# Optimization experiments

Measured on AMD Instinct MI355X. Metric: run time of the kernel, lower is better.

## Reference

```python
import jax, jax.numpy as jnp
import numpy as np

EPS = 1e-5

def _segment_mean(src_feat, edge_index, num_targets):
    # src_feat: [Ns, D]; edge_index: [2, E] = [source_idx, target_idx]
    msgs = src_feat[edge_index[0]]                                   # [E, D] gather
    agg = jax.ops.segment_sum(msgs, edge_index[1], num_segments=num_targets)
    deg = jax.ops.segment_sum(jnp.ones((edge_index.shape[1],), src_feat.dtype),
                              edge_index[1], num_segments=num_targets)
    return agg / jnp.clip(deg, 1.0)[:, None]

def _layernorm(x, gamma, beta):
    mu = jnp.mean(x, axis=-1, keepdims=True)
    var = jnp.mean(jnp.square(x - mu), axis=-1, keepdims=True)
    return (x - mu) * jax.lax.rsqrt(var + EPS) * gamma + beta

def setup_inputs() -> dict:
    key = jax.random.key(0)
    ks = jax.random.split(key, 8)
    NU, NI, E, D = 50000, 50000, 300000, 256
    s = 1.0 / np.sqrt(D)
    return {
        "user_features": jax.random.normal(ks[0], (NU, D), jnp.float32),
        "item_features": jax.random.normal(ks[1], (NI, D), jnp.float32),
        "user_item_edge_index": jax.random.randint(ks[2], (2, E), 0, NI),
        "item_user_edge_index": jax.random.randint(ks[3], (2, E), 0, NU),
        "Wu": jax.random.uniform(ks[4], (D, D), jnp.float32, -s, s),
        "bu": jax.random.uniform(ks[5], (D,), jnp.float32, -s, s),
        "Wi": jax.random.uniform(ks[6], (D, D), jnp.float32, -s, s),
        "bi": jax.random.uniform(ks[7], (D,), jnp.float32, -s, s),
        "gamma": jnp.ones((D,), jnp.float32),
        "beta": jnp.zeros((D,), jnp.float32),
    }

def reference(user_features, item_features, user_item_edge_index, item_user_edge_index,
              Wu, bu, Wi, bi, gamma, beta):
    num_items = item_features.shape[0]
    num_users = user_features.shape[0]
    # messages into items come from users; into users come from items
    item_messages = _segment_mean(user_features, user_item_edge_index, num_items)
    user_messages = _segment_mean(item_features, item_user_edge_index, num_users)
    u_new = (user_features + user_messages) @ Wu + bu
    i_new = (item_features + item_messages) @ Wi + bi
    u_new = _layernorm(jax.nn.relu(u_new), gamma, beta)
    i_new = _layernorm(jax.nn.relu(i_new), gamma, beta)
    return (u_new, i_new)
```

## Files before the change

kernel.cpp:

```cpp
#include <hip/hip_runtime.h>
#include <hip/hip_bf16.h>

#define D 256
#define BM 64
#define LDA 264
#define LDAF 260
#define LDK 72

typedef __attribute__((ext_vector_type(8))) __bf16 bf16x8;
typedef __attribute__((ext_vector_type(4))) float f32x4;

__device__ __forceinline__ float bf2f(unsigned short u) {
    union { unsigned int i; float f; } c; c.i = ((unsigned int)u) << 16; return c.f;
}
__device__ __forceinline__ float bf2f_lo(unsigned int u) {
    union { unsigned int i; float f; } c; c.i = u << 16; return c.f;
}
__device__ __forceinline__ float bf2f_hi(unsigned int u) {
    union { unsigned int i; float f; } c; c.i = u & 0xffff0000u; return c.f;
}
__device__ __forceinline__ unsigned short f2bf(float f) {
    __hip_bfloat16 h = __float2bfloat16(f);
    return *reinterpret_cast<unsigned short*>(&h);
}
__device__ __forceinline__ unsigned int pack2(float lo, float hi) {
    return (unsigned int)f2bf(lo) | ((unsigned int)f2bf(hi) << 16);
}


__global__ void k_prep(const float* __restrict__ uf, const float* __restrict__ itf,
                       const float* __restrict__ Wu, const float* __restrict__ Wi,
                       unsigned short* __restrict__ feat_bf,
                       unsigned short* __restrict__ Wt_u, unsigned short* __restrict__ Wt_i,
                       const int* __restrict__ iu_e, int Eiu,
                       const int* __restrict__ ui_e, int Eui,
                       int* __restrict__ deg, int NU,
                       size_t nfU, size_t nfTot, int nbF) {
    int b = blockIdx.x;
    if (b < nbF) {
        size_t base = ((size_t)b * 256 + threadIdx.x) * 8;
        if (base < nfTot) {
            const float* s = (base < nfU) ? (uf + base) : (itf + (base - nfU));
            float4 f0 = *(const float4*)s;
            float4 f1 = *(const float4*)(s + 4);
            ushort4 o0, o1;
            o0.x = f2bf(f0.x); o0.y = f2bf(f0.y); o0.z = f2bf(f0.z); o0.w = f2bf(f0.w);
            o1.x = f2bf(f1.x); o1.y = f2bf(f1.y); o1.z = f2bf(f1.z); o1.w = f2bf(f1.w);
            ((ushort4*)(feat_bf + base))[0] = o0;
            ((ushort4*)(feat_bf + base))[1] = o1;
        }
    } else if (b < nbF + 512) {
        int b2 = b - nbF;
        const float* W = (b2 < 256) ? Wu : Wi;
        unsigned short* Wt = (b2 < 256) ? Wt_u : Wt_i;
        int k = b2 & 255;
        int c = threadIdx.x;
        Wt[(size_t)c * 256 + k] = f2bf(W[(size_t)k * 256 + c]);
    } else {
        int e = (b - nbF - 512) * 256 + threadIdx.x;
        if (e < Eiu) {
            atomicAdd(&deg[iu_e[Eiu + e]], 1);
        } else if (e < Eiu + Eui) {
            int e2 = e - Eiu;
            atomicAdd(&deg[NU + ui_e[Eui + e2]], 1);
        }
    }
}

__global__ void k_scan_block(const int* __restrict__ deg, int N,
                             int* __restrict__ rs, int* __restrict__ bsums) {
    __shared__ int s[1024];
    int base = blockIdx.x * 1024;
    int t = threadIdx.x;
    int v = (base + t < N) ? deg[base + t] : 0;
    s[t] = v;
    __syncthreads();
    for (int off = 1; off < 1024; off <<= 1) {
        int add = (t >= off) ? s[t - off] : 0;
        __syncthreads();
        s[t] += add;
        __syncthreads();
    }
    if (base + t < N) rs[base + t + 1] = s[t];
    if (t == 1023) bsums[blockIdx.x] = s[1023];
}

__global__ void k_scan_sums(int* __restrict__ bsums, int nb) {
    __shared__ int s[1024];
    int t = threadIdx.x;
    int v = (t < nb) ? bsums[t] : 0;
    s[t] = v;
    __syncthreads();
    for (int off = 1; off < 1024; off <<= 1) {
        int add = (t >= off) ? s[t - off] : 0;
        __syncthreads();
        s[t] += add;
        __syncthreads();
    }
    if (t < nb) bsums[t] = s[t] - v;
}

__global__ void k_finalize(int N, int* __restrict__ rs, int* __restrict__ cur,
                           const int* __restrict__ bsums) {
    int i = blockIdx.x * blockDim.x + threadIdx.x;
    if (i < N) {
        int v = rs[i + 1] + bsums[i >> 10];
        rs[i + 1] = v;
        cur[i + 1] = v;
    }
    if (i == 0) { rs[0] = 0; cur[0] = 0; }
}

__global__ void k_fill2(const int* __restrict__ iu_e, int Eiu,
                        const int* __restrict__ ui_e, int Eui,
                        int* __restrict__ cur, int NU,
                        int* __restrict__ csr) {
    int e = blockIdx.x * blockDim.x + threadIdx.x;
    if (e < Eiu) {
        int d = iu_e[Eiu + e];
        int p = atomicAdd(&cur[d], 1);
        csr[p] = iu_e[e];
    } else if (e < Eiu + Eui) {
        int e2 = e - Eiu;
        int d = ui_e[Eui + e2];
        int p = atomicAdd(&cur[NU + d], 1);
        csr[p] = ui_e[e2];
    }
}

__launch_bounds__(256)
__global__ void k_fused(const unsigned short* __restrict__ uf_bf,
                        const unsigned short* __restrict__ if_bf,
                        const unsigned short* __restrict__ Wt_u,
                        const unsigned short* __restrict__ Wt_i,
                        const int* __restrict__ rs, const int* __restrict__ csr,
                        const float* __restrict__ bu, const float* __restrict__ bi,
                        const float* __restrict__ gamma, const float* __restrict__ beta,
                        int NU, int NI, int nbU, float* __restrict__ out) {
    __shared__ __align__(16) __hip_bfloat16 As[BM][LDA];
    __shared__ float red_s[BM][4];
    __shared__ float red_q[BM][4];

    int b = blockIdx.x;
    bool isU = b < nbU;
    const unsigned short* srcT = isU ? if_bf : uf_bf;
    const unsigned short* tgtT = isU ? uf_bf : if_bf;
    const unsigned short* Wt   = isU ? Wt_u : Wt_i;
    const float* bias          = isU ? bu : bi;
    float* Y                   = isU ? out : out + (size_t)NU * D;
    int N                      = isU ? NU : NI;
    int row0 = (isU ? b : b - nbU) * BM;
    int wvBase = (isU ? 0 : NU) + row0;

    int t = threadIdx.x;
    int lane = t & 63;
    int w = t >> 6;
    int l15 = lane & 15;
    int l4 = lane >> 4;
    int half = lane >> 5;
    int hl = lane & 31;

    for (int it = 0; it < 8; ++it) {
        int lrow = (it * 4 + w) * 2 + half;
        int grow = row0 + lrow;
        if (grow < N) {
            int wv = wvBase + lrow;
            int s0 = rs[wv], s1 = rs[wv + 1];
            float a0[8] = {}, a1[8] = {}, a2[8] = {}, a3[8] = {};
            int i = s0;
            for (; i + 4 <= s1; i += 4) {
                int e0 = csr[i], e1 = csr[i + 1], e2 = csr[i + 2], e3 = csr[i + 3];
                uint4 r0 = ((const uint4*)(srcT + (size_t)e0 * D))[hl];
                uint4 r1 = ((const uint4*)(srcT + (size_t)e1 * D))[hl];
                uint4 r2 = ((const uint4*)(srcT + (size_t)e2 * D))[hl];
                uint4 r3 = ((const uint4*)(srcT + (size_t)e3 * D))[hl];
                a0[0] += bf2f_lo(r0.x); a0[1] += bf2f_hi(r0.x); a0[2] += bf2f_lo(r0.y); a0[3] += bf2f_hi(r0.y);
                a0[4] += bf2f_lo(r0.z); a0[5] += bf2f_hi(r0.z); a0[6] += bf2f_lo(r0.w); a0[7] += bf2f_hi(r0.w);
                a1[0] += bf2f_lo(r1.x); a1[1] += bf2f_hi(r1.x); a1[2] += bf2f_lo(r1.y); a1[3] += bf2f_hi(r1.y);
                a1[4] += bf2f_lo(r1.z); a1[5] += bf2f_hi(r1.z); a1[6] += bf2f_lo(r1.w); a1[7] += bf2f_hi(r1.w);
                a2[0] += bf2f_lo(r2.x); a2[1] += bf2f_hi(r2.x); a2[2] += bf2f_lo(r2.y); a2[3] += bf2f_hi(r2.y);
                a2[4] += bf2f_lo(r2.z); a2[5] += bf2f_hi(r2.z); a2[6] += bf2f_lo(r2.w); a2[7] += bf2f_hi(r2.w);
                a3[0] += bf2f_lo(r3.x); a3[1] += bf2f_hi(r3.x); a3[2] += bf2f_lo(r3.y); a3[3] += bf2f_hi(r3.y);
                a3[4] += bf2f_lo(r3.z); a3[5] += bf2f_hi(r3.z); a3[6] += bf2f_lo(r3.w); a3[7] += bf2f_hi(r3.w);
            }
            for (; i < s1; ++i) {
                int e0 = csr[i];
                uint4 r0 = ((const uint4*)(srcT + (size_t)e0 * D))[hl];
                a0[0] += bf2f_lo(r0.x); a0[1] += bf2f_hi(r0.x); a0[2] += bf2f_lo(r0.y); a0[3] += bf2f_hi(r0.y);
                a0[4] += bf2f_lo(r0.z); a0[5] += bf2f_hi(r0.z); a0[6] += bf2f_lo(r0.w); a0[7] += bf2f_hi(r0.w);
            }
            int cnt = s1 - s0;
            float inv = 1.0f / (float)(cnt > 0 ? cnt : 1);
            uint4 tv = ((const uint4*)(tgtT + (size_t)grow * D))[hl];
            float x0 = bf2f_lo(tv.x) + (a0[0] + a1[0] + a2[0] + a3[0]) * inv;
            float x1 = bf2f_hi(tv.x) + (a0[1] + a1[1] + a2[1] + a3[1]) * inv;
            float x2 = bf2f_lo(tv.y) + (a0[2] + a1[2] + a2[2] + a3[2]) * inv;
            float x3 = bf2f_hi(tv.y) + (a0[3] + a1[3] + a2[3] + a3[3]) * inv;
            float x4 = bf2f_lo(tv.z) + (a0[4] + a1[4] + a2[4] + a3[4]) * inv;
            float x5 = bf2f_hi(tv.z) + (a0[5] + a1[5] + a2[5] + a3[5]) * inv;
            float x6 = bf2f_lo(tv.w) + (a0[6] + a1[6] + a2[6] + a3[6]) * inv;
            float x7 = bf2f_hi(tv.w) + (a0[7] + a1[7] + a2[7] + a3[7]) * inv;
            uint4 o;
            o.x = pack2(x0, x1); o.y = pack2(x2, x3); o.z = pack2(x4, x5); o.w = pack2(x6, x7);
            *(uint4*)&As[lrow][hl * 8] = o;
        } else {
            uint4 z = {0, 0, 0, 0};
            *(uint4*)&As[lrow][hl * 8] = z;
        }
    }

    f32x4 acc[4][4];
    f32x4 zero = {0.f, 0.f, 0.f, 0.f};
    #pragma unroll
    for (int fr = 0; fr < 4; fr++)
        #pragma unroll
        for (int fc = 0; fc < 4; fc++)
            acc[fr][fc] = zero;

    __syncthreads();

    const uint4* Bg = (const uint4*)Wt;
    int colB = w * 64 + l15;
    #pragma unroll
    for (int ks8 = 0; ks8 < 8; ++ks8) {
        uint4 bq[4];
        #pragma unroll
        for (int fc = 0; fc < 4; ++fc)
            bq[fc] = Bg[(size_t)(colB + fc * 16) * 32 + ks8 * 4 + l4];
        bf16x8 af[4];
        #pragma unroll
        for (int fr = 0; fr < 4; ++fr)
            af[fr] = *(const bf16x8*)&As[fr * 16 + l15][ks8 * 32 + l4 * 8];
        #pragma unroll
        for (int fr = 0; fr < 4; ++fr)
            #pragma unroll
            for (int fc = 0; fc < 4; ++fc)
                acc[fr][fc] = __builtin_amdgcn_mfma_f32_16x16x32_bf16(
                    af[fr], *(bf16x8*)&bq[fc], acc[fr][fc], 0, 0, 0);
    }

    float bias_c[4], gam_c[4], bet_c[4];
    #pragma unroll
    for (int fc = 0; fc < 4; fc++) {
        int col = w * 64 + fc * 16 + l15;
        bias_c[fc] = bias[col];
        gam_c[fc]  = gamma[col];
        bet_c[fc]  = beta[col];
    }

    #pragma unroll
    for (int fr = 0; fr < 4; fr++) {
        #pragma unroll
        for (int r = 0; r < 4; r++) {
            int row = fr * 16 + l4 * 4 + r;
            float s = 0.f, q = 0.f;
            #pragma unroll
            for (int fc = 0; fc < 4; fc++) {
                float v = acc[fr][fc][r] + bias_c[fc];
                v = fmaxf(v, 0.f);
                acc[fr][fc][r] = v;
                s += v;
                q += v * v;
            }
            #pragma unroll
            for (int m = 1; m < 16; m <<= 1) {
                s += __shfl_xor(s, m);
                q += __shfl_xor(q, m);
            }
            if (l15 == 0) { red_s[row][w] = s; red_q[row][w] = q; }
        }
    }
    __syncthreads();

    float* AsF = (float*)&As[0][0];
    for (int h = 0; h < 2; ++h) {
        #pragma unroll
        for (int fr2 = 0; fr2 < 2; ++fr2) {
            int fr = h * 2 + fr2;
            #pragma unroll
            for (int r = 0; r < 4; ++r) {
                int row = fr * 16 + l4 * 4 + r;
                float s = red_s[row][0] + red_s[row][1] + red_s[row][2] + red_s[row][3];
                float q = red_q[row][0] + red_q[row][1] + red_q[row][2] + red_q[row][3];
                float mu  = s * (1.0f / 256.0f);
                float var = q * (1.0f / 256.0f) - mu * mu;
                float rstd = rsqrtf(var + 1e-5f);
                int lr = row - h * 32;
                #pragma unroll
                for (int fc = 0; fc < 4; ++fc) {
                    int col = w * 64 + fc * 16 + l15;
                    AsF[lr * LDAF + col] = (acc[fr][fc][r] - mu) * rstd * gam_c[fc] + bet_c[fc];
                }
            }
        }
        __syncthreads();
        #pragma unroll
        for (int j = 0; j < 8; ++j) {
            int r = j * 4 + w;
            int grow = row0 + h * 32 + r;
            if (grow < N) {
                float4 v = *(float4*)&AsF[r * LDAF + lane * 4];
                *(float4*)&Y[(size_t)grow * D + lane * 4] = v;
            }
        }
        __syncthreads();
    }
}


__global__ void k_hist(const int* __restrict__ dst, int E, int* __restrict__ deg) {
    int e = blockIdx.x * blockDim.x + threadIdx.x;
    if (e < E) atomicAdd(&deg[dst[e]], 1);
}

__global__ void k_finalize_rs(int N, int* __restrict__ rs, const int* __restrict__ bsums) {
    int i = blockIdx.x * blockDim.x + threadIdx.x;
    if (i < N) rs[i + 1] += bsums[i >> 10];
    if (i == 0) rs[0] = 0;
}

__global__ void k_fill(const int* __restrict__ src, const int* __restrict__ dst, int E,
                       const int* __restrict__ rs, int* __restrict__ cursor,
                       int* __restrict__ csr) {
    int e = blockIdx.x * blockDim.x + threadIdx.x;
    if (e < E) {
        int d = dst[e];
        int p = atomicAdd(&cursor[d], 1);
        csr[rs[d] + p] = src[e];
    }
}

__global__ void k_msg_x(const float* __restrict__ srcf, const float* __restrict__ tgtf,
                        const int* __restrict__ rs, const int* __restrict__ csr,
                        int N, float* __restrict__ xout) {
    int wave = (blockIdx.x * blockDim.x + threadIdx.x) >> 6;
    int lane = threadIdx.x & 63;
    if (wave >= N) return;
    int s0 = rs[wave], s1 = rs[wave + 1];
    float4 acc = make_float4(0.f, 0.f, 0.f, 0.f);
    for (int i = s0; i < s1; i++) {
        int s = csr[i];
        float4 f = *(const float4*)&srcf[(size_t)s * D + lane * 4];
        acc.x += f.x; acc.y += f.y; acc.z += f.z; acc.w += f.w;
    }
    int cnt = s1 - s0;
    float inv = 1.0f / (float)(cnt > 0 ? cnt : 1);
    float4 t = *(const float4*)&tgtf[(size_t)wave * D + lane * 4];
    float4 x;
    x.x = t.x + acc.x * inv;
    x.y = t.y + acc.y * inv;
    x.z = t.z + acc.z * inv;
    x.w = t.w + acc.w * inv;
    *(float4*)&xout[(size_t)wave * D + lane * 4] = x;
}

__global__ void k_wcvt(const float* __restrict__ W0, const float* __restrict__ W1,
                       __hip_bfloat16* __restrict__ Wt0, __hip_bfloat16* __restrict__ Wt1) {
    int b = blockIdx.x;
    const float* W = (b < 256) ? W0 : W1;
    __hip_bfloat16* Wt = (b < 256) ? Wt0 : Wt1;
    int k = b & 255;
    int c = threadIdx.x;
    Wt[(size_t)c * 256 + k] = __float2bfloat16(W[(size_t)k * 256 + c]);
}

__launch_bounds__(256)
__global__ void k_gemm_mfma_ln(const float* __restrict__ X,
                               const __hip_bfloat16* __restrict__ Wt,
                               const float* __restrict__ bias,
                               const float* __restrict__ gamma,
                               const float* __restrict__ beta,
                               int N, float* __restrict__ Y) {
    __shared__ __hip_bfloat16 As[BM][LDK];
    __shared__ __hip_bfloat16 Bs[D][LDK];
    __shared__ float red_s[BM][4];
    __shared__ float red_q[BM][4];

    int t = threadIdx.x;
    int lane = t & 63;
    int w = t >> 6;
    int l15 = lane & 15;
    int l4 = lane >> 4;
    int row0 = blockIdx.x * BM;

    f32x4 acc[4][4];
    f32x4 zero = {0.f, 0.f, 0.f, 0.f};
    #pragma unroll
    for (int fr = 0; fr < 4; fr++)
        #pragma unroll
        for (int fc = 0; fc < 4; fc++)
            acc[fr][fc] = zero;

    for (int k0 = 0; k0 < D; k0 += 64) {
        {
            int i = t >> 2;
            int kq = (t & 3) * 16;
            int r = row0 + i;
            float4 f[4];
            if (r < N) {
                const float4* p = (const float4*)&X[(size_t)r * D + k0 + kq];
                f[0] = p[0]; f[1] = p[1]; f[2] = p[2]; f[3] = p[3];
            } else {
                float4 z4 = make_float4(0.f, 0.f, 0.f, 0.f);
                f[0] = z4; f[1] = z4; f[2] = z4; f[3] = z4;
            }
            __hip_bfloat16 vb[16];
            #pragma unroll
            for (int q = 0; q < 4; q++) {
                vb[q * 4 + 0] = __float2bfloat16(f[q].x);
                vb[q * 4 + 1] = __float2bfloat16(f[q].y);
                vb[q * 4 + 2] = __float2bfloat16(f[q].z);
                vb[q * 4 + 3] = __float2bfloat16(f[q].w);
            }
            *(uint4*)&As[i][kq]     = *(uint4*)&vb[0];
            *(uint4*)&As[i][kq + 8] = *(uint4*)&vb[8];
        }
        #pragma unroll
        for (int pass = 0; pass < 4; pass++) {
            int c = pass * 64 + (t >> 2);
            int kq = (t & 3) * 16;
            const uint4* p = (const uint4*)&Wt[(size_t)c * D + k0 + kq];
            uint4 b0 = p[0], b1 = p[1];
            *(uint4*)&Bs[c][kq]     = b0;
            *(uint4*)&Bs[c][kq + 8] = b1;
        }
        __syncthreads();

        #pragma unroll
        for (int ks = 0; ks < 2; ks++) {
            bf16x8 af[4], bg[4];
            #pragma unroll
            for (int fr = 0; fr < 4; fr++)
                af[fr] = *(const bf16x8*)&As[fr * 16 + l15][ks * 32 + l4 * 8];
            #pragma unroll
            for (int fc = 0; fc < 4; fc++)
                bg[fc] = *(const bf16x8*)&Bs[w * 64 + fc * 16 + l15][ks * 32 + l4 * 8];
            #pragma unroll
            for (int fr = 0; fr < 4; fr++)
                #pragma unroll
                for (int fc = 0; fc < 4; fc++)
                    acc[fr][fc] = __builtin_amdgcn_mfma_f32_16x16x32_bf16(
                        af[fr], bg[fc], acc[fr][fc], 0, 0, 0);
        }
        __syncthreads();
    }

    float bias_c[4], gam_c[4], bet_c[4];
    #pragma unroll
    for (int fc = 0; fc < 4; fc++) {
        int col = w * 64 + fc * 16 + l15;
        bias_c[fc] = bias[col];
        gam_c[fc]  = gamma[col];
        bet_c[fc]  = beta[col];
    }

    #pragma unroll
    for (int fr = 0; fr < 4; fr++) {
        #pragma unroll
        for (int r = 0; r < 4; r++) {
            int row = fr * 16 + l4 * 4 + r;
            float s = 0.f, q = 0.f;
            #pragma unroll
            for (int fc = 0; fc < 4; fc++) {
                float v = acc[fr][fc][r] + bias_c[fc];
                v = fmaxf(v, 0.f);
                acc[fr][fc][r] = v;
                s += v;
                q += v * v;
            }
            #pragma unroll
            for (int m = 1; m < 16; m <<= 1) {
                s += __shfl_xor(s, m);
                q += __shfl_xor(q, m);
            }
            if (l15 == 0) { red_s[row][w] = s; red_q[row][w] = q; }
        }
    }
    __syncthreads();

    #pragma unroll
    for (int fr = 0; fr < 4; fr++) {
        #pragma unroll
        for (int r = 0; r < 4; r++) {
            int row = fr * 16 + l4 * 4 + r;
            int grow = row0 + row;
            if (grow >= N) continue;
            float s = red_s[row][0] + red_s[row][1] + red_s[row][2] + red_s[row][3];
            float q = red_q[row][0] + red_q[row][1] + red_q[row][2] + red_q[row][3];
            float mu  = s * (1.0f / 256.0f);
            float var = q * (1.0f / 256.0f) - mu * mu;
            float rstd = rsqrtf(var + 1e-5f);
            #pragma unroll
            for (int fc = 0; fc < 4; fc++) {
                int col = w * 64 + fc * 16 + l15;
                Y[(size_t)grow * D + col] = (acc[fr][fc][r] - mu) * rstd * gam_c[fc] + bet_c[fc];
            }
        }
    }
}


extern "C" void kernel_launch(void* const* d_in, const int* in_sizes, int n_in,
                              void* d_out, int out_size, void* d_ws, size_t ws_size,
                              hipStream_t stream) {
    const float* uf    = (const float*)d_in[0];
    const float* itf   = (const float*)d_in[1];
    const int*   ui_e  = (const int*)d_in[2];
    const int*   iu_e  = (const int*)d_in[3];
    const float* Wu    = (const float*)d_in[4];
    const float* bu    = (const float*)d_in[5];
    const float* Wi    = (const float*)d_in[6];
    const float* bi    = (const float*)d_in[7];
    const float* gamma = (const float*)d_in[8];
    const float* beta  = (const float*)d_in[9];

    int NU  = in_sizes[0] / D;
    int NI  = in_sizes[1] / D;
    int Eui = in_sizes[2] / 2;
    int Eiu = in_sizes[3] / 2;
    int Nmax = NU > NI ? NU : NI;
    int Ntot = NU + NI;
    int Etot = Eiu + Eui;

    float* out   = (float*)d_out;
    size_t nfU = (size_t)NU * D;
    size_t nfI = (size_t)NI * D;
    size_t nfTot = nfU + nfI;

    unsigned short* uf_bf = (unsigned short*)d_ws;
    unsigned short* if_bf = uf_bf + nfU;
    unsigned short* Wt_u2 = if_bf + nfI;
    unsigned short* Wt_i2 = Wt_u2 + 65536;
    int* deg2  = (int*)(Wt_i2 + 65536);
    int* rs2   = deg2 + Ntot;
    int* cur2  = rs2 + Ntot + 1;
    int* bsums = cur2 + Ntot + 1;
    int* csr2  = bsums + 1024;
    size_t needed = (size_t)((char*)(csr2 + Etot) - (char*)d_ws);

    if (ws_size >= needed) {
        int nbF = (int)((nfTot + 2047) / 2048);
        int nbH = (Etot + 255) / 256;
        hipMemsetAsync(deg2, 0, (size_t)Ntot * sizeof(int), stream);
        k_prep<<<nbF + 512 + nbH, 256, 0, stream>>>(uf, itf, Wu, Wi, uf_bf, Wt_u2, Wt_i2,
                                                    iu_e, Eiu, ui_e, Eui, deg2, NU,
                                                    nfU, nfTot, nbF);
        int nb = (Ntot + 1023) / 1024;
        k_scan_block<<<nb, 1024, 0, stream>>>(deg2, Ntot, rs2, bsums);
        k_scan_sums<<<1, 1024, 0, stream>>>(bsums, nb);
        k_finalize<<<(Ntot + 255) / 256, 256, 0, stream>>>(Ntot, rs2, cur2, bsums);
        k_fill2<<<nbH, 256, 0, stream>>>(iu_e, Eiu, ui_e, Eui, cur2, NU, csr2);
        int nbU = (NU + BM - 1) / BM;
        int nbI = (NI + BM - 1) / BM;
        k_fused<<<nbU + nbI, 256, 0, stream>>>(uf_bf, if_bf, Wt_u2, Wt_i2, rs2, csr2,
                                               bu, bi, gamma, beta, NU, NI, nbU, out);
        return;
    }

    float* u_out = out;
    float* i_out = out + nfU;
    __hip_bfloat16* Wt_u = (__hip_bfloat16*)d_ws;
    __hip_bfloat16* Wt_i = Wt_u + 256 * 256;
    int* deg    = (int*)(Wt_i + 256 * 256);
    int* rs     = deg + Nmax;
    int* bs     = rs + Nmax + 1;
    int* cursor = bs + 1024;
    int* csr    = cursor + Nmax;

    k_wcvt<<<512, 256, 0, stream>>>(Wu, Wi, Wt_u, Wt_i);

    auto run_side = [&](const float* srcf, const float* tgtf, const int* edges, int E,
                        int N, const __hip_bfloat16* Wt, const float* bias, float* y) {
        const int* esrc = edges;
        const int* edst = edges + E;
        hipMemsetAsync(deg, 0, (size_t)N * sizeof(int), stream);
        hipMemsetAsync(cursor, 0, (size_t)N * sizeof(int), stream);
        k_hist<<<(E + 255) / 256, 256, 0, stream>>>(edst, E, deg);
        int nb = (N + 1023) / 1024;
        k_scan_block<<<nb, 1024, 0, stream>>>(deg, N, rs, bs);
        k_scan_sums<<<1, 1024, 0, stream>>>(bs, nb);
        k_finalize_rs<<<(N + 255) / 256, 256, 0, stream>>>(N, rs, bs);
        k_fill<<<(E + 255) / 256, 256, 0, stream>>>(esrc, edst, E, rs, cursor, csr);
        k_msg_x<<<(N + 3) / 4, 256, 0, stream>>>(srcf, tgtf, rs, csr, N, y);
        k_gemm_mfma_ln<<<(N + BM - 1) / BM, 256, 0, stream>>>(y, Wt, bias, gamma, beta, N, y);
    };

    run_side(itf, uf, iu_e, Eiu, NU, Wt_u, bu, u_out);
    run_side(uf, itf, ui_e, Eui, NI, Wt_i, bi, i_out);
}
```

Before: 240.9 us.

## Split gather-mean aggregation into separate kernel before GEMM+LayerNorm

```diff
diff --git a/kernel.cpp b/kernel.cpp
--- a/kernel.cpp
+++ b/kernel.cpp
@@ -128,12 +128,70 @@
     }
 }
 
+__global__ void k_msg2(const unsigned short* __restrict__ uf_bf,
+                       const unsigned short* __restrict__ if_bf,
+                       const int* __restrict__ rs, const int* __restrict__ csr,
+                       unsigned short* __restrict__ x_u, unsigned short* __restrict__ x_i,
+                       int NU, int NI) {
+    int pair = (blockIdx.x * blockDim.x + threadIdx.x) >> 6;
+    int lane = threadIdx.x & 63;
+    int half = lane >> 5;
+    int hl   = lane & 31;
+    int Ntot = NU + NI;
+    int wv = pair * 2 + half;
+    if (wv >= Ntot) return;
+
+    const unsigned short* src; const unsigned short* tgt; unsigned short* xo; int w;
+    if (wv < NU) { src = if_bf; tgt = uf_bf; xo = x_u; w = wv; }
+    else         { src = uf_bf; tgt = if_bf; xo = x_i; w = wv - NU; }
+
+    int s0 = rs[wv], s1 = rs[wv + 1];
+    float a0[8] = {}, a1[8] = {}, a2[8] = {}, a3[8] = {};
+
+    int i = s0;
+    for (; i + 4 <= s1; i += 4) {
+        int e0 = csr[i], e1 = csr[i + 1], e2 = csr[i + 2], e3 = csr[i + 3];
+        uint4 r0 = ((const uint4*)(src + (size_t)e0 * D))[hl];
+        uint4 r1 = ((const uint4*)(src + (size_t)e1 * D))[hl];
+        uint4 r2 = ((const uint4*)(src + (size_t)e2 * D))[hl];
+        uint4 r3 = ((const uint4*)(src + (size_t)e3 * D))[hl];
+        a0[0] += bf2f_lo(r0.x); a0[1] += bf2f_hi(r0.x); a0[2] += bf2f_lo(r0.y); a0[3] += bf2f_hi(r0.y);
+        a0[4] += bf2f_lo(r0.z); a0[5] += bf2f_hi(r0.z); a0[6] += bf2f_lo(r0.w); a0[7] += bf2f_hi(r0.w);
+        a1[0] += bf2f_lo(r1.x); a1[1] += bf2f_hi(r1.x); a1[2] += bf2f_lo(r1.y); a1[3] += bf2f_hi(r1.y);
+        a1[4] += bf2f_lo(r1.z); a1[5] += bf2f_hi(r1.z); a1[6] += bf2f_lo(r1.w); a1[7] += bf2f_hi(r1.w);
+        a2[0] += bf2f_lo(r2.x); a2[1] += bf2f_hi(r2.x); a2[2] += bf2f_lo(r2.y); a2[3] += bf2f_hi(r2.y);
+        a2[4] += bf2f_lo(r2.z); a2[5] += bf2f_hi(r2.z); a2[6] += bf2f_lo(r2.w); a2[7] += bf2f_hi(r2.w);
+        a3[0] += bf2f_lo(r3.x); a3[1] += bf2f_hi(r3.x); a3[2] += bf2f_lo(r3.y); a3[3] += bf2f_hi(r3.y);
+        a3[4] += bf2f_lo(r3.z); a3[5] += bf2f_hi(r3.z); a3[6] += bf2f_lo(r3.w); a3[7] += bf2f_hi(r3.w);
+    }
+    for (; i < s1; ++i) {
+        int e0 = csr[i];
+        uint4 r0 = ((const uint4*)(src + (size_t)e0 * D))[hl];
+        a0[0] += bf2f_lo(r0.x); a0[1] += bf2f_hi(r0.x); a0[2] += bf2f_lo(r0.y); a0[3] += bf2f_hi(r0.y);
+        a0[4] += bf2f_lo(r0.z); a0[5] += bf2f_hi(r0.z); a0[6] += bf2f_lo(r0.w); a0[7] += bf2f_hi(r0.w);
+    }
+
+    int cnt = s1 - s0;
+    float inv = 1.0f / (float)(cnt > 0 ? cnt : 1);
+    uint4 tv = ((const uint4*)(tgt + (size_t)w * D))[hl];
+    float x0 = bf2f_lo(tv.x) + (a0[0] + a1[0] + a2[0] + a3[0]) * inv;
+    float x1 = bf2f_hi(tv.x) + (a0[1] + a1[1] + a2[1] + a3[1]) * inv;
+    float x2 = bf2f_lo(tv.y) + (a0[2] + a1[2] + a2[2] + a3[2]) * inv;
+    float x3 = bf2f_hi(tv.y) + (a0[3] + a1[3] + a2[3] + a3[3]) * inv;
+    float x4 = bf2f_lo(tv.z) + (a0[4] + a1[4] + a2[4] + a3[4]) * inv;
+    float x5 = bf2f_hi(tv.z) + (a0[5] + a1[5] + a2[5] + a3[5]) * inv;
+    float x6 = bf2f_lo(tv.w) + (a0[6] + a1[6] + a2[6] + a3[6]) * inv;
+    float x7 = bf2f_hi(tv.w) + (a0[7] + a1[7] + a2[7] + a3[7]) * inv;
+    uint4 o;
+    o.x = pack2(x0, x1); o.y = pack2(x2, x3); o.z = pack2(x4, x5); o.w = pack2(x6, x7);
+    ((uint4*)(xo + (size_t)w * D))[hl] = o;
+}
+
 __launch_bounds__(256)
-__global__ void k_fused(const unsigned short* __restrict__ uf_bf,
-                        const unsigned short* __restrict__ if_bf,
+__global__ void k_gemm3(const unsigned short* __restrict__ x_u,
+                        const unsigned short* __restrict__ x_i,
                         const unsigned short* __restrict__ Wt_u,
                         const unsigned short* __restrict__ Wt_i,
-                        const int* __restrict__ rs, const int* __restrict__ csr,
                         const float* __restrict__ bu, const float* __restrict__ bi,
                         const float* __restrict__ gamma, const float* __restrict__ beta,
                         int NU, int NI, int nbU, float* __restrict__ out) {
@@ -143,69 +201,27 @@
 
     int b = blockIdx.x;
     bool isU = b < nbU;
-    const unsigned short* srcT = isU ? if_bf : uf_bf;
-    const unsigned short* tgtT = isU ? uf_bf : if_bf;
-    const unsigned short* Wt   = isU ? Wt_u : Wt_i;
-    const float* bias          = isU ? bu : bi;
-    float* Y                   = isU ? out : out + (size_t)NU * D;
-    int N                      = isU ? NU : NI;
+    const unsigned short* X  = isU ? x_u : x_i;
+    const unsigned short* Wt = isU ? Wt_u : Wt_i;
+    const float* bias        = isU ? bu : bi;
+    float* Y                 = isU ? out : out + (size_t)NU * D;
+    int N                    = isU ? NU : NI;
     int row0 = (isU ? b : b - nbU) * BM;
-    int wvBase = (isU ? 0 : NU) + row0;
 
     int t = threadIdx.x;
     int lane = t & 63;
     int w = t >> 6;
     int l15 = lane & 15;
     int l4 = lane >> 4;
-    int half = lane >> 5;
-    int hl = lane & 31;
-
-    for (int it = 0; it < 8; ++it) {
-        int lrow = (it * 4 + w) * 2 + half;
-        int grow = row0 + lrow;
-        if (grow < N) {
-            int wv = wvBase + lrow;
-            int s0 = rs[wv], s1 = rs[wv + 1];
-            float a0[8] = {}, a1[8] = {}, a2[8] = {}, a3[8] = {};
-            int i = s0;
-            for (; i + 4 <= s1; i += 4) {
-                int e0 = csr[i], e1 = csr[i + 1], e2 = csr[i + 2], e3 = csr[i + 3];
-                uint4 r0 = ((const uint4*)(srcT + (size_t)e0 * D))[hl];
-                uint4 r1 = ((const uint4*)(srcT + (size_t)e1 * D))[hl];
-                uint4 r2 = ((const uint4*)(srcT + (size_t)e2 * D))[hl];
-                uint4 r3 = ((const uint4*)(srcT + (size_t)e3 * D))[hl];
-                a0[0] += bf2f_lo(r0.x); a0[1] += bf2f_hi(r0.x); a0[2] += bf2f_lo(r0.y); a0[3] += bf2f_hi(r0.y);
-                a0[4] += bf2f_lo(r0.z); a0[5] += bf2f_hi(r0.z); a0[6] += bf2f_lo(r0.w); a0[7] += bf2f_hi(r0.w);
-                a1[0] += bf2f_lo(r1.x); a1[1] += bf2f_hi(r1.x); a1[2] += bf2f_lo(r1.y); a1[3] += bf2f_hi(r1.y);
-                a1[4] += bf2f_lo(r1.z); a1[5] += bf2f_hi(r1.z); a1[6] += bf2f_lo(r1.w); a1[7] += bf2f_hi(r1.w);
-                a2[0] += bf2f_lo(r2.x); a2[1] += bf2f_hi(r2.x); a2[2] += bf2f_lo(r2.y); a2[3] += bf2f_hi(r2.y);
-                a2[4] += bf2f_lo(r2.z); a2[5] += bf2f_hi(r2.z); a2[6] += bf2f_lo(r2.w); a2[7] += bf2f_hi(r2.w);
-                a3[0] += bf2f_lo(r3.x); a3[1] += bf2f_hi(r3.x); a3[2] += bf2f_lo(r3.y); a3[3] += bf2f_hi(r3.y);
-                a3[4] += bf2f_lo(r3.z); a3[5] += bf2f_hi(r3.z); a3[6] += bf2f_lo(r3.w); a3[7] += bf2f_hi(r3.w);
-            }
-            for (; i < s1; ++i) {
-                int e0 = csr[i];
-                uint4 r0 = ((const uint4*)(srcT + (size_t)e0 * D))[hl];
-                a0[0] += bf2f_lo(r0.x); a0[1] += bf2f_hi(r0.x); a0[2] += bf2f_lo(r0.y); a0[3] += bf2f_hi(r0.y);
-                a0[4] += bf2f_lo(r0.z); a0[5] += bf2f_hi(r0.z); a0[6] += bf2f_lo(r0.w); a0[7] += bf2f_hi(r0.w);
-            }
-            int cnt = s1 - s0;
-            float inv = 1.0f / (float)(cnt > 0 ? cnt : 1);
-            uint4 tv = ((const uint4*)(tgtT + (size_t)grow * D))[hl];
-            float x0 = bf2f_lo(tv.x) + (a0[0] + a1[0] + a2[0] + a3[0]) * inv;
-            float x1 = bf2f_hi(tv.x) + (a0[1] + a1[1] + a2[1] + a3[1]) * inv;
-            float x2 = bf2f_lo(tv.y) + (a0[2] + a1[2] + a2[2] + a3[2]) * inv;
-            float x3 = bf2f_hi(tv.y) + (a0[3] + a1[3] + a2[3] + a3[3]) * inv;
-            float x4 = bf2f_lo(tv.z) + (a0[4] + a1[4] + a2[4] + a3[4]) * inv;
-            float x5 = bf2f_hi(tv.z) + (a0[5] + a1[5] + a2[5] + a3[5]) * inv;
-            float x6 = bf2f_lo(tv.w) + (a0[6] + a1[6] + a2[6] + a3[6]) * inv;
-            float x7 = bf2f_hi(tv.w) + (a0[7] + a1[7] + a2[7] + a3[7]) * inv;
-            uint4 o;
-            o.x = pack2(x0, x1); o.y = pack2(x2, x3); o.z = pack2(x4, x5); o.w = pack2(x6, x7);
-            *(uint4*)&As[lrow][hl * 8] = o;
-        } else {
-            uint4 z = {0, 0, 0, 0};
-            *(uint4*)&As[lrow][hl * 8] = z;
+
+    {
+        const uint4* Xg = (const uint4*)&X[(size_t)row0 * D];
+        #pragma unroll
+        for (int j = 0; j < 8; ++j) {
+            int lr = (t >> 5) + j * 8;
+            uint4 v = {0, 0, 0, 0};
+            if (row0 + lr < N) v = Xg[(size_t)lr * 32 + (t & 31)];
+            *(uint4*)&As[lr][(t & 31) * 8] = v;
         }
     }
 
@@ -529,7 +545,9 @@
 
     unsigned short* uf_bf = (unsigned short*)d_ws;
     unsigned short* if_bf = uf_bf + nfU;
-    unsigned short* Wt_u2 = if_bf + nfI;
+    unsigned short* x_u   = if_bf + nfI;
+    unsigned short* x_i   = x_u + nfU;
+    unsigned short* Wt_u2 = x_i + nfI;
     unsigned short* Wt_i2 = Wt_u2 + 65536;
     int* deg2  = (int*)(Wt_i2 + 65536);
     int* rs2   = deg2 + Ntot;
@@ -550,10 +568,12 @@
         k_scan_sums<<<1, 1024, 0, stream>>>(bsums, nb);
         k_finalize<<<(Ntot + 255) / 256, 256, 0, stream>>>(Ntot, rs2, cur2, bsums);
         k_fill2<<<nbH, 256, 0, stream>>>(iu_e, Eiu, ui_e, Eui, cur2, NU, csr2);
+        int pairs = (Ntot + 1) / 2;
+        k_msg2<<<(pairs + 3) / 4, 256, 0, stream>>>(uf_bf, if_bf, rs2, csr2, x_u, x_i, NU, NI);
         int nbU = (NU + BM - 1) / BM;
         int nbI = (NI + BM - 1) / BM;
-        k_fused<<<nbU + nbI, 256, 0, stream>>>(uf_bf, if_bf, Wt_u2, Wt_i2, rs2, csr2,
-                                               bu, bi, gamma, beta, NU, NI, nbU, out);
+        k_gemm3<<<nbU + nbI, 256, 0, stream>>>(x_u, x_i, Wt_u2, Wt_i2, bu, bi, gamma, beta,
+                                               NU, NI, nbU, out);
         return;
     }
 
```

New measurement: 226.3 us. 6.1% less time.

## Shrink fused aggregate-GEMM-LayerNorm tile to 16 rows with 512-thread blocks

Applied to the files above, without the earlier changes.

```diff
diff --git a/kernel.cpp b/kernel.cpp
--- a/kernel.cpp
+++ b/kernel.cpp
@@ -3,8 +3,8 @@
 
 #define D 256
 #define BM 64
+#define BMF 16
 #define LDA 264
-#define LDAF 260
 #define LDK 72
 
 typedef __attribute__((ext_vector_type(8))) __bf16 bf16x8;
@@ -128,18 +128,18 @@
     }
 }
 
-__launch_bounds__(256)
-__global__ void k_fused(const unsigned short* __restrict__ uf_bf,
-                        const unsigned short* __restrict__ if_bf,
-                        const unsigned short* __restrict__ Wt_u,
-                        const unsigned short* __restrict__ Wt_i,
-                        const int* __restrict__ rs, const int* __restrict__ csr,
-                        const float* __restrict__ bu, const float* __restrict__ bi,
-                        const float* __restrict__ gamma, const float* __restrict__ beta,
-                        int NU, int NI, int nbU, float* __restrict__ out) {
-    __shared__ __align__(16) __hip_bfloat16 As[BM][LDA];
-    __shared__ float red_s[BM][4];
-    __shared__ float red_q[BM][4];
+__launch_bounds__(512)
+__global__ void k_fused2(const unsigned short* __restrict__ uf_bf,
+                         const unsigned short* __restrict__ if_bf,
+                         const unsigned short* __restrict__ Wt_u,
+                         const unsigned short* __restrict__ Wt_i,
+                         const int* __restrict__ rs, const int* __restrict__ csr,
+                         const float* __restrict__ bu, const float* __restrict__ bi,
+                         const float* __restrict__ gamma, const float* __restrict__ beta,
+                         int NU, int NI, int nbU, float* __restrict__ out) {
+    __shared__ __align__(16) __hip_bfloat16 As[BMF][LDA];
+    __shared__ float red_s[BMF][8];
+    __shared__ float red_q[BMF][8];
 
     int b = blockIdx.x;
     bool isU = b < nbU;
@@ -149,19 +149,19 @@
     const float* bias          = isU ? bu : bi;
     float* Y                   = isU ? out : out + (size_t)NU * D;
     int N                      = isU ? NU : NI;
-    int row0 = (isU ? b : b - nbU) * BM;
+    int row0 = (isU ? b : b - nbU) * BMF;
     int wvBase = (isU ? 0 : NU) + row0;
 
     int t = threadIdx.x;
+    int w = t >> 6;
     int lane = t & 63;
-    int w = t >> 6;
+    int half = lane >> 5;
+    int hl = lane & 31;
     int l15 = lane & 15;
     int l4 = lane >> 4;
-    int half = lane >> 5;
-    int hl = lane & 31;
-
-    for (int it = 0; it < 8; ++it) {
-        int lrow = (it * 4 + w) * 2 + half;
+
+    {
+        int lrow = w * 2 + half;
         int grow = row0 + lrow;
         if (grow < N) {
             int wv = wvBase + lrow;
@@ -209,101 +209,70 @@
         }
     }
 
-    f32x4 acc[4][4];
+    __syncthreads();
+
+    const uint4* Bg = (const uint4*)Wt;
+    f32x4 acc[2];
     f32x4 zero = {0.f, 0.f, 0.f, 0.f};
-    #pragma unroll
-    for (int fr = 0; fr < 4; fr++)
-        #pragma unroll
-        for (int fc = 0; fc < 4; fc++)
-            acc[fr][fc] = zero;
-
-    __syncthreads();
-
-    const uint4* Bg = (const uint4*)Wt;
-    int colB = w * 64 + l15;
+    acc[0] = zero; acc[1] = zero;
     #pragma unroll
     for (int ks8 = 0; ks8 < 8; ++ks8) {
-        uint4 bq[4];
-        #pragma unroll
-        for (int fc = 0; fc < 4; ++fc)
-            bq[fc] = Bg[(size_t)(colB + fc * 16) * 32 + ks8 * 4 + l4];
-        bf16x8 af[4];
-        #pragma unroll
-        for (int fr = 0; fr < 4; ++fr)
-            af[fr] = *(const bf16x8*)&As[fr * 16 + l15][ks8 * 32 + l4 * 8];
-        #pragma unroll
-        for (int fr = 0; fr < 4; ++fr)
-            #pragma unroll
-            for (int fc = 0; fc < 4; ++fc)
-                acc[fr][fc] = __builtin_amdgcn_mfma_f32_16x16x32_bf16(
-                    af[fr], *(bf16x8*)&bq[fc], acc[fr][fc], 0, 0, 0);
-    }
-
-    float bias_c[4], gam_c[4], bet_c[4];
-    #pragma unroll
-    for (int fc = 0; fc < 4; fc++) {
-        int col = w * 64 + fc * 16 + l15;
+        bf16x8 af = *(const bf16x8*)&As[l15][ks8 * 32 + l4 * 8];
+        #pragma unroll
+        for (int fc = 0; fc < 2; ++fc) {
+            uint4 bq = Bg[(size_t)(w * 32 + fc * 16 + l15) * 32 + ks8 * 4 + l4];
+            acc[fc] = __builtin_amdgcn_mfma_f32_16x16x32_bf16(
+                af, *(bf16x8*)&bq, acc[fc], 0, 0, 0);
+        }
+    }
+
+    float bias_c[2], gam_c[2], bet_c[2];
+    #pragma unroll
+    for (int fc = 0; fc < 2; ++fc) {
+        int col = w * 32 + fc * 16 + l15;
         bias_c[fc] = bias[col];
         gam_c[fc]  = gamma[col];
         bet_c[fc]  = beta[col];
     }
 
     #pragma unroll
-    for (int fr = 0; fr < 4; fr++) {
-        #pragma unroll
-        for (int r = 0; r < 4; r++) {
-            int row = fr * 16 + l4 * 4 + r;
-            float s = 0.f, q = 0.f;
-            #pragma unroll
-            for (int fc = 0; fc < 4; fc++) {
-                float v = acc[fr][fc][r] + bias_c[fc];
-                v = fmaxf(v, 0.f);
-                acc[fr][fc][r] = v;
-                s += v;
-                q += v * v;
-            }
-            #pragma unroll
-            for (int m = 1; m < 16; m <<= 1) {
-                s += __shfl_xor(s, m);
-                q += __shfl_xor(q, m);
-            }
-            if (l15 == 0) { red_s[row][w] = s; red_q[row][w] = q; }
-        }
+    for (int r = 0; r < 4; ++r) {
+        int row = l4 * 4 + r;
+        float s = 0.f, q = 0.f;
+        #pragma unroll
+        for (int fc = 0; fc < 2; ++fc) {
+            float v = acc[fc][r] + bias_c[fc];
+            v = fmaxf(v, 0.f);
+            acc[fc][r] = v;
+            s += v;
+            q += v * v;
+        }
+        #pragma unroll
+        for (int m = 1; m < 16; m <<= 1) {
+            s += __shfl_xor(s, m);
+            q += __shfl_xor(q, m);
+        }
+        if (l15 == 0) { red_s[row][w] = s; red_q[row][w] = q; }
     }
     __syncthreads();
 
-    float* AsF = (float*)&As[0][0];
-    for (int h = 0; h < 2; ++h) {
-        #pragma unroll
-        for (int fr2 = 0; fr2 < 2; ++fr2) {
-            int fr = h * 2 + fr2;
-            #pragma unroll
-            for (int r = 0; r < 4; ++r) {
-                int row = fr * 16 + l4 * 4 + r;
-                float s = red_s[row][0] + red_s[row][1] + red_s[row][2] + red_s[row][3];
-                float q = red_q[row][0] + red_q[row][1] + red_q[row][2] + red_q[row][3];
-                float mu  = s * (1.0f / 256.0f);
-                float var = q * (1.0f / 256.0f) - mu * mu;
-                float rstd = rsqrtf(var + 1e-5f);
-                int lr = row - h * 32;
-                #pragma unroll
-                for (int fc = 0; fc < 4; ++fc) {
-                    int col = w * 64 + fc * 16 + l15;
-                    AsF[lr * LDAF + col] = (acc[fr][fc][r] - mu) * rstd * gam_c[fc] + bet_c[fc];
-                }
-            }
-        }
-        __syncthreads();
-        #pragma unroll
-        for (int j = 0; j < 8; ++j) {
-            int r = j * 4 + w;
-            int grow = row0 + h * 32 + r;
-            if (grow < N) {
-                float4 v = *(float4*)&AsF[r * LDAF + lane * 4];
-                *(float4*)&Y[(size_t)grow * D + lane * 4] = v;
-            }
-        }
-        __syncthreads();
+    #pragma unroll
+    for (int r = 0; r < 4; ++r) {
+        int row = l4 * 4 + r;
+        int grow = row0 + row;
+        if (grow >= N) continue;
+        float s = red_s[row][0] + red_s[row][1] + red_s[row][2] + red_s[row][3]
+                + red_s[row][4] + red_s[row][5] + red_s[row][6] + red_s[row][7];
+        float q = red_q[row][0] + red_q[row][1] + red_q[row][2] + red_q[row][3]
+                + red_q[row][4] + red_q[row][5] + red_q[row][6] + red_q[row][7];
+        float mu  = s * (1.0f / 256.0f);
+        float var = q * (1.0f / 256.0f) - mu * mu;
+        float rstd = rsqrtf(var + 1e-5f);
+        #pragma unroll
+        for (int fc = 0; fc < 2; ++fc) {
+            int col = w * 32 + fc * 16 + l15;
+            Y[(size_t)grow * D + col] = (acc[fc][r] - mu) * rstd * gam_c[fc] + bet_c[fc];
+        }
     }
 }
 
@@ -550,10 +519,10 @@
         k_scan_sums<<<1, 1024, 0, stream>>>(bsums, nb);
         k_finalize<<<(Ntot + 255) / 256, 256, 0, stream>>>(Ntot, rs2, cur2, bsums);
         k_fill2<<<nbH, 256, 0, stream>>>(iu_e, Eiu, ui_e, Eui, cur2, NU, csr2);
-        int nbU = (NU + BM - 1) / BM;
-        int nbI = (NI + BM - 1) / BM;
-        k_fused<<<nbU + nbI, 256, 0, stream>>>(uf_bf, if_bf, Wt_u2, Wt_i2, rs2, csr2,
-                                               bu, bi, gamma, beta, NU, NI, nbU, out);
+        int nbU = (NU + BMF - 1) / BMF;
+        int nbI = (NI + BMF - 1) / BMF;
+        k_fused2<<<nbU + nbI, 512, 0, stream>>>(uf_bf, if_bf, Wt_u2, Wt_i2, rs2, csr2,
+                                                bu, bi, gamma, beta, NU, NI, nbU, out);
         return;
     }
 
```

Result: slower. 260.9 us (+8.3%).
